# Performance work log

Hardware: AMD Instinct MI355X
Metric: run time of the kernel (lower is better)

The kernel has to match this reference:

```python
import jax, jax.numpy as jnp
import numpy as np

D_MODEL = 1024
STATE_DIM = 128


def setup_inputs() -> dict:
    key = jax.random.key(0)
    ks = jax.random.split(key, 8)
    B, T, D, N = 8, 4096, D_MODEL, STATE_DIM
    u = jax.random.normal(ks[0], (B, T, D), dtype=jnp.float32)
    h0 = jnp.zeros((B, N), dtype=jnp.float32)
    log_A = jax.random.normal(ks[1], (N,), dtype=jnp.float32) * 0.1 - 1.0
    B_w = jax.random.normal(ks[2], (N, D), dtype=jnp.float32) / np.sqrt(D)
    B_b = jax.random.normal(ks[3], (N,), dtype=jnp.float32) * 0.01
    C_w = jax.random.normal(ks[4], (D, N), dtype=jnp.float32) / np.sqrt(N)
    C_b = jax.random.normal(ks[5], (D,), dtype=jnp.float32) * 0.01
    D_param = jnp.ones((D,), dtype=jnp.float32) * 0.1
    log_dt = jax.random.normal(ks[6], (N,), dtype=jnp.float32) * 0.1 - 2.0
    return {"u": u, "h0": h0, "log_A": log_A, "B_w": B_w, "B_b": B_b,
            "C_w": C_w, "C_b": C_b, "D_param": D_param, "log_dt": log_dt}


def reference(u, h0, log_A, B_w, B_b, C_w, C_b, D_param, log_dt):
    # u: [B, T, D], h0: [B, N]
    dt = jnp.minimum(jnp.exp(log_dt), 1.0)          # [N]
    A = -jnp.exp(log_A)                             # [N]
    A_bar = jnp.exp(A * dt)                         # [N]
    # B_bar * u, precomputed for all timesteps: [B, T, N]
    Bu = (jnp.einsum('btd,nd->btn', u, B_w) + B_b) * dt

    def step(h, bu_t):
        h = A_bar * h + bu_t                        # [B, N]
        return h, h

    # scan over time: Bu transposed to [T, B, N]
    _, hs = jax.lax.scan(step, h0, jnp.swapaxes(Bu, 0, 1))
    hs = jnp.swapaxes(hs, 0, 1)                     # [B, T, N]
    # y = C h + c_bias + D * u
    y = jnp.einsum('btn,dn->btd', hs, C_w) + C_b + D_param * u
    return y
```

## Files before the change

kernel.cpp:

```cpp
#include <hip/hip_runtime.h>

#define B_SZ 8
#define T_SZ 4096
#define D_SZ 1024
#define N_SZ 128
#define M_SZ (B_SZ*T_SZ)
#define CHUNK 64
#define NCHUNK (T_SZ/CHUNK)

typedef __attribute__((ext_vector_type(8))) __bf16 bf16x8;
typedef __attribute__((ext_vector_type(4))) float f32x4;
typedef __attribute__((ext_vector_type(4))) unsigned int u32x4;
typedef __attribute__((ext_vector_type(4))) float fvec4;

static __device__ __forceinline__ unsigned short f2bf(float f){
  union { float f; unsigned int u; } v; v.f = f;
  unsigned int r = v.u + 0x7fffu + ((v.u >> 16) & 1u);
  return (unsigned short)(r >> 16);
}

static __device__ __forceinline__ void cp16(const void* g, void* l){
  __builtin_amdgcn_global_load_lds(
      (const __attribute__((address_space(1))) void*)g,
      (__attribute__((address_space(3))) void*)l, 16, 0, 0);
}

static __device__ __forceinline__ f32x4 zero4(){
  f32x4 v = {0.f, 0.f, 0.f, 0.f};
  return v;
}

__global__ __launch_bounds__(256) void k_conv(const float* __restrict__ Bw,
                                              const float* __restrict__ Cw,
                                              unsigned short* __restrict__ bw,
                                              unsigned short* __restrict__ cw){
  int t = blockIdx.x*256 + threadIdx.x;
  {
    int n = t >> 10, k = t & 1023;
    int c = k >> 6, kk = k & 63;
    unsigned byte = (unsigned)c*16384u + (unsigned)n*128u
                  + (unsigned)((kk*2) ^ ((n&7)<<4));
    bw[byte>>1] = f2bf(Bw[n*1024 + k]);
  }
  {
    int d = t >> 7, k = t & 127;
    int c = d >> 7, dd = d & 127;
    unsigned byte = (unsigned)c*32768u + (unsigned)dd*256u
                  + (unsigned)((k*2) ^ ((dd&15)<<4));
    cw[byte>>1] = f2bf(Cw[d*128 + k]);
  }
}

__global__ __launch_bounds__(256) void k_gemm1c(const float* __restrict__ u,
                                                const unsigned short* __restrict__ bw,
                                                const float* __restrict__ Bb,
                                                const float* __restrict__ logA,
                                                const float* __restrict__ logdt,
                                                float* __restrict__ Bu,
                                                float* __restrict__ carry){
  __shared__ __align__(16) char smem[32768];
  unsigned short* lA = (unsigned short*)smem;
  unsigned short* lB = (unsigned short*)(smem + 8192);
  float*          BuT = (float*)smem;
  const int tid  = threadIdx.x;
  const int lane = tid & 63;
  const int wave = tid >> 6;
  const int bc   = blockIdx.x;
  const int m0   = bc * 64;
  const int l15  = lane & 15;
  const int lhi  = lane >> 4;

  f32x4 acc[8];
  #pragma unroll
  for (int i=0;i<8;++i) acc[i] = zero4();

  for (int kc=0; kc<16; ++kc){
    #pragma unroll
    for (int rep=0; rep<4; ++rep){
      const char* g = (const char*)bw + kc*16384 + rep*4096 + wave*1024 + lane*16;
      char* l = (char*)lB + rep*4096 + wave*1024;
      cp16(g, l);
    }
    #pragma unroll
    for (int rep=0; rep<2; ++rep){
      int q = rep*256 + tid;
      int row = q >> 3, ks = q & 7;
      const float* src = u + (size_t)(m0+row)*1024 + kc*64 + ks*8;
      fvec4 f0 = *(const fvec4*)src;
      fvec4 f1 = *(const fvec4*)(src+4);
      u32x4 p;
      p.x = (unsigned)f2bf(f0.x) | ((unsigned)f2bf(f0.y)<<16);
      p.y = (unsigned)f2bf(f0.z) | ((unsigned)f2bf(f0.w)<<16);
      p.z = (unsigned)f2bf(f1.x) | ((unsigned)f2bf(f1.y)<<16);
      p.w = (unsigned)f2bf(f1.z) | ((unsigned)f2bf(f1.w)<<16);
      unsigned byte = (unsigned)row*128u + (unsigned)((ks*16) ^ ((row&7)<<4));
      *(u32x4*)((char*)lA + byte) = p;
    }
    __syncthreads();
    #pragma unroll
    for (int k0=0; k0<64; k0+=32){
      int arow = wave*16 + l15;
      int ak = k0 + lhi*8;
      bf16x8 af = *(const bf16x8*)((const char*)lA + arow*128 + ((ak*2) ^ ((arow&7)<<4)));
      #pragma unroll
      for (int ct=0; ct<8; ++ct){
        int bn = ct*16 + l15;
        bf16x8 bfv = *(const bf16x8*)((const char*)lB + bn*128 + ((ak*2) ^ ((bn&7)<<4)));
        acc[ct] = __builtin_amdgcn_mfma_f32_16x16x32_bf16(af, bfv, acc[ct], 0, 0, 0);
      }
    }
    __syncthreads();
  }

  #pragma unroll
  for (int ct=0; ct<8; ++ct){
    int n = ct*16 + l15;
    float dt = fminf(__expf(logdt[n]), 1.f);
    float bb = Bb[n];
    #pragma unroll
    for (int r=0;r<4;++r){
      int ml = wave*16 + lhi*4 + r;
      BuT[ml*128 + n] = (acc[ct][r] + bb) * dt;
    }
  }
  __syncthreads();

  fvec4* dst = (fvec4*)(Bu + (size_t)bc*64*128);
  const fvec4* srcT = (const fvec4*)BuT;
  #pragma unroll
  for (int i=0;i<8;++i){
    int idx = i*256 + tid;
    dst[idx] = srcT[idx];
  }

  if (tid < 128){
    int n = tid;
    float dt = fminf(__expf(logdt[n]), 1.f);
    float Ab = __expf(-__expf(logA[n]) * dt);
    float h = 0.f;
    #pragma unroll 8
    for (int j=0;j<CHUNK;++j) h = fmaf(Ab, h, BuT[j*128 + n]);
    carry[(size_t)bc*128 + n] = h;
  }
}

__global__ __launch_bounds__(128) void k_scan_pref(const float* __restrict__ carry,
                                                   const float* __restrict__ h0,
                                                   float* __restrict__ hin,
                                                   const float* __restrict__ logA,
                                                   const float* __restrict__ logdt){
  int b = blockIdx.x;
  int n = threadIdx.x;
  float dt = fminf(__expf(logdt[n]), 1.f);
  float Ad = -__expf(logA[n]) * dt;
  float AL = __expf(Ad * (float)CHUNK);
  float h = h0[b*128 + n];
  hin[(size_t)(b*NCHUNK)*128 + n] = h;
  #pragma unroll 8
  for (int c=1;c<NCHUNK;++c){
    h = fmaf(AL, h, carry[(size_t)(b*NCHUNK + c - 1)*128 + n]);
    hin[(size_t)(b*NCHUNK + c)*128 + n] = h;
  }
}

__global__ __launch_bounds__(256) void k_gemm2s(const float* __restrict__ Bu,
                                                const float* __restrict__ hin,
                                                const unsigned short* __restrict__ cw,
                                                const float* __restrict__ u,
                                                const float* __restrict__ Cb,
                                                const float* __restrict__ Dp,
                                                const float* __restrict__ logA,
                                                const float* __restrict__ logdt,
                                                float* __restrict__ y){
  __shared__ __align__(16) float          BuT[64*128];
  __shared__ __align__(16) unsigned short hsT[64*128];
  __shared__ __align__(16) unsigned short cwT[128*128];
  const int tid = threadIdx.x, lane = tid & 63, wave = tid >> 6;
  const int bc = blockIdx.x;
  const int m0 = bc * 64;
  const int l15 = lane & 15, lhi = lane >> 4;

  if (wave < 2){
    #pragma unroll
    for (int i=0;i<16;++i){
      int off = (wave*16 + i)*1024 + lane*16;
      cp16((const char*)Bu + (size_t)bc*32768 + off, (char*)BuT + off);
    }
  } else {
    #pragma unroll
    for (int i=0;i<16;++i){
      int off = ((wave-2)*16 + i)*1024 + lane*16;
      cp16((const char*)cw + off, (char*)cwT + off);
    }
  }
  __syncthreads();

  if (tid < 128){
    int n = tid;
    float dt = fminf(__expf(logdt[n]), 1.f);
    float Ab = __expf(-__expf(logA[n]) * dt);
    float h = hin[(size_t)bc*128 + n];
    #pragma unroll 8
    for (int j=0;j<CHUNK;++j){
      h = fmaf(Ab, h, BuT[j*128 + n]);
      unsigned byte = (unsigned)j*256u + (unsigned)((n*2) ^ ((j&15)<<4));
      *(unsigned short*)((char*)hsT + byte) = f2bf(h);
    }
  }
  __syncthreads();

  for (int d=0; d<8; ++d){
    f32x4 acc[8];
    #pragma unroll
    for (int i=0;i<8;++i) acc[i] = zero4();

    #pragma unroll
    for (int k0=0;k0<128;k0+=32){
      int arow = wave*16 + l15;
      int ak = k0 + lhi*8;
      bf16x8 af = *(const bf16x8*)((const char*)hsT + arow*256 + ((ak*2) ^ ((arow&15)<<4)));
      #pragma unroll
      for (int ct=0;ct<8;++ct){
        int dn = ct*16 + l15;
        bf16x8 bfv = *(const bf16x8*)((const char*)cwT + dn*256 + ((ak*2) ^ ((dn&15)<<4)));
        acc[ct] = __builtin_amdgcn_mfma_f32_16x16x32_bf16(af, bfv, acc[ct], 0, 0, 0);
      }
    }
    __syncthreads();

    if (d < 7){
      #pragma unroll
      for (int i=0;i<8;++i){
        int off = (wave*8 + i)*1024 + lane*16;
        cp16((const char*)cw + (size_t)(d+1)*32768 + off, (char*)cwT + off);
      }
    }

    const int d0 = d*128;
    #pragma unroll
    for (int ct=0;ct<8;++ct){
      int dc = d0 + ct*16 + l15;
      float cb = Cb[dc], dp = Dp[dc];
      #pragma unroll
      for (int r=0;r<4;++r){
        int m = m0 + wave*16 + lhi*4 + r;
        size_t off = (size_t)m*1024 + dc;
        y[off] = acc[ct][r] + cb + dp*u[off];
      }
    }
    __syncthreads();
  }
}

extern "C" void kernel_launch(void* const* d_in, const int* in_sizes, int n_in,
                              void* d_out, int out_size, void* d_ws, size_t ws_size,
                              hipStream_t stream){
  (void)in_sizes; (void)n_in; (void)out_size; (void)ws_size;
  const float* u     = (const float*)d_in[0];
  const float* h0    = (const float*)d_in[1];
  const float* logA  = (const float*)d_in[2];
  const float* Bw    = (const float*)d_in[3];
  const float* Bb    = (const float*)d_in[4];
  const float* Cw    = (const float*)d_in[5];
  const float* Cb    = (const float*)d_in[6];
  const float* Dp    = (const float*)d_in[7];
  const float* logdt = (const float*)d_in[8];
  float* y = (float*)d_out;

  char* ws = (char*)d_ws;
  float*          Bu    = (float*)(ws);
  float*          carry = (float*)(ws + 16777216);
  float*          hin   = (float*)(ws + 17039360);
  unsigned short* bw    = (unsigned short*)(ws + 17301504);
  unsigned short* cw    = (unsigned short*)(ws + 17563648);

  k_conv      <<<dim3(512), dim3(256), 0, stream>>>(Bw, Cw, bw, cw);
  k_gemm1c    <<<dim3(512), dim3(256), 0, stream>>>(u, bw, Bb, logA, logdt, Bu, carry);
  k_scan_pref <<<dim3(8),   dim3(128), 0, stream>>>(carry, h0, hin, logA, logdt);
  k_gemm2s    <<<dim3(512), dim3(256), 0, stream>>>(Bu, hin, cw, u, Cb, Dp, logA, logdt, y);
}
```

Measured before the change: 91.60 us.

## Store Bu intermediate in bf16 and fold chunk-prefix scan into second GEMM

The Bu intermediate written by the first GEMM is now packed to bf16, halving its global write and read traffic and the LDS footprint in the second kernel. The separate serial prefix-scan kernel is removed. Each block of the second kernel recomputes its incoming state by scanning the carries of all earlier chunks in its batch, overlapped with the async LDS loads. This removes one launch and the 8-block serial kernel, but adds up to 63 dependent carry loads per block and lowers the precision of Bu before the recurrence.

```diff
diff --git a/kernel.cpp b/kernel.cpp
--- a/kernel.cpp
+++ b/kernel.cpp
@@ -17,6 +17,11 @@
   union { float f; unsigned int u; } v; v.f = f;
   unsigned int r = v.u + 0x7fffu + ((v.u >> 16) & 1u);
   return (unsigned short)(r >> 16);
+}
+
+static __device__ __forceinline__ float bf2f(unsigned short s){
+  union { unsigned int u; float f; } v; v.u = ((unsigned)s) << 16;
+  return v.f;
 }
 
 static __device__ __forceinline__ void cp16(const void* g, void* l){
@@ -56,7 +61,7 @@
                                                 const float* __restrict__ Bb,
                                                 const float* __restrict__ logA,
                                                 const float* __restrict__ logdt,
-                                                float* __restrict__ Bu,
+                                                unsigned short* __restrict__ Bu_bf,
                                                 float* __restrict__ carry){
   __shared__ __align__(16) char smem[32768];
   unsigned short* lA = (unsigned short*)smem;
@@ -125,12 +130,18 @@
   }
   __syncthreads();
 
-  fvec4* dst = (fvec4*)(Bu + (size_t)bc*64*128);
-  const fvec4* srcT = (const fvec4*)BuT;
-  #pragma unroll
-  for (int i=0;i<8;++i){
-    int idx = i*256 + tid;
-    dst[idx] = srcT[idx];
+  #pragma unroll
+  for (int i=0;i<4;++i){
+    int q = i*256 + tid;
+    const float* s = BuT + q*8;
+    fvec4 a = *(const fvec4*)s;
+    fvec4 b = *(const fvec4*)(s+4);
+    u32x4 p;
+    p.x = (unsigned)f2bf(a.x) | ((unsigned)f2bf(a.y)<<16);
+    p.y = (unsigned)f2bf(a.z) | ((unsigned)f2bf(a.w)<<16);
+    p.z = (unsigned)f2bf(b.x) | ((unsigned)f2bf(b.y)<<16);
+    p.w = (unsigned)f2bf(b.z) | ((unsigned)f2bf(b.w)<<16);
+    *(u32x4*)((char*)Bu_bf + (size_t)bc*16384 + (size_t)q*16) = p;
   }
 
   if (tid < 128){
@@ -144,35 +155,17 @@
   }
 }
 
-__global__ __launch_bounds__(128) void k_scan_pref(const float* __restrict__ carry,
-                                                   const float* __restrict__ h0,
-                                                   float* __restrict__ hin,
-                                                   const float* __restrict__ logA,
-                                                   const float* __restrict__ logdt){
-  int b = blockIdx.x;
-  int n = threadIdx.x;
-  float dt = fminf(__expf(logdt[n]), 1.f);
-  float Ad = -__expf(logA[n]) * dt;
-  float AL = __expf(Ad * (float)CHUNK);
-  float h = h0[b*128 + n];
-  hin[(size_t)(b*NCHUNK)*128 + n] = h;
-  #pragma unroll 8
-  for (int c=1;c<NCHUNK;++c){
-    h = fmaf(AL, h, carry[(size_t)(b*NCHUNK + c - 1)*128 + n]);
-    hin[(size_t)(b*NCHUNK + c)*128 + n] = h;
-  }
-}
-
-__global__ __launch_bounds__(256) void k_gemm2s(const float* __restrict__ Bu,
-                                                const float* __restrict__ hin,
+__global__ __launch_bounds__(256) void k_gemm2s(const unsigned short* __restrict__ Bu_bf,
+                                                const float* __restrict__ carry,
                                                 const unsigned short* __restrict__ cw,
                                                 const float* __restrict__ u,
+                                                const float* __restrict__ h0,
                                                 const float* __restrict__ Cb,
                                                 const float* __restrict__ Dp,
                                                 const float* __restrict__ logA,
                                                 const float* __restrict__ logdt,
                                                 float* __restrict__ y){
-  __shared__ __align__(16) float          BuT[64*128];
+  __shared__ __align__(16) unsigned short BuT[64*128];
   __shared__ __align__(16) unsigned short hsT[64*128];
   __shared__ __align__(16) unsigned short cwT[128*128];
   const int tid = threadIdx.x, lane = tid & 63, wave = tid >> 6;
@@ -180,29 +173,38 @@
   const int m0 = bc * 64;
   const int l15 = lane & 15, lhi = lane >> 4;
 
-  if (wave < 2){
-    #pragma unroll
-    for (int i=0;i<16;++i){
-      int off = (wave*16 + i)*1024 + lane*16;
-      cp16((const char*)Bu + (size_t)bc*32768 + off, (char*)BuT + off);
-    }
-  } else {
-    #pragma unroll
-    for (int i=0;i<16;++i){
-      int off = ((wave-2)*16 + i)*1024 + lane*16;
-      cp16((const char*)cw + off, (char*)cwT + off);
-    }
-  }
-  __syncthreads();
-
+  #pragma unroll
+  for (int i=0;i<4;++i){
+    int off = i*4096 + tid*16;
+    cp16((const char*)Bu_bf + (size_t)bc*16384 + off, (char*)BuT + off);
+  }
+  #pragma unroll
+  for (int i=0;i<8;++i){
+    int off = i*4096 + tid*16;
+    cp16((const char*)cw + off, (char*)cwT + off);
+  }
+
+  float hreg = 0.f, Ab = 0.f;
   if (tid < 128){
     int n = tid;
+    int b = bc >> 6, c = bc & 63;
     float dt = fminf(__expf(logdt[n]), 1.f);
-    float Ab = __expf(-__expf(logA[n]) * dt);
-    float h = hin[(size_t)bc*128 + n];
+    float Ad = -__expf(logA[n]) * dt;
+    Ab = __expf(Ad);
+    float AL = __expf(Ad * (float)CHUNK);
+    float h = h0[b*128 + n];
+    for (int i=0;i<c;++i)
+      h = fmaf(AL, h, carry[(size_t)(b*NCHUNK + i)*128 + n]);
+    hreg = h;
+  }
+  __syncthreads();
+
+  if (tid < 128){
+    int n = tid;
+    float h = hreg;
     #pragma unroll 8
     for (int j=0;j<CHUNK;++j){
-      h = fmaf(Ab, h, BuT[j*128 + n]);
+      h = fmaf(Ab, h, bf2f(BuT[j*128 + n]));
       unsigned byte = (unsigned)j*256u + (unsigned)((n*2) ^ ((j&15)<<4));
       *(unsigned short*)((char*)hsT + byte) = f2bf(h);
     }
@@ -268,14 +270,13 @@
   float* y = (float*)d_out;
 
   char* ws = (char*)d_ws;
-  float*          Bu    = (float*)(ws);
-  float*          carry = (float*)(ws + 16777216);
-  float*          hin   = (float*)(ws + 17039360);
-  unsigned short* bw    = (unsigned short*)(ws + 17301504);
-  unsigned short* cw    = (unsigned short*)(ws + 17563648);
-
-  k_conv      <<<dim3(512), dim3(256), 0, stream>>>(Bw, Cw, bw, cw);
-  k_gemm1c    <<<dim3(512), dim3(256), 0, stream>>>(u, bw, Bb, logA, logdt, Bu, carry);
-  k_scan_pref <<<dim3(8),   dim3(128), 0, stream>>>(carry, h0, hin, logA, logdt);
-  k_gemm2s    <<<dim3(512), dim3(256), 0, stream>>>(Bu, hin, cw, u, Cb, Dp, logA, logdt, y);
-}
+  unsigned short* Bu_bf = (unsigned short*)(ws);
+  float*          carry = (float*)(ws + 8388608);
+  unsigned short* bw    = (unsigned short*)(ws + 8650752);
+  unsigned short* cw    = (unsigned short*)(ws + 8912896);
+
+  k_conv  <<<dim3(512), dim3(256), 0, stream>>>(Bw, Cw, bw, cw);
+  k_gemm1c<<<dim3(512), dim3(256), 0, stream>>>(u, bw, Bb, logA, logdt, Bu_bf, carry);
+  k_gemm2s<<<dim3(512), dim3(256), 0, stream>>>(Bu_bf, carry, cw, u, h0, Cb, Dp,
+                                                logA, logdt, y);
+}
```

Result: faster. 87.88 us (-4.1%).
